# Performance work log

Hardware: AMD Instinct MI355X
Metric: run time of the kernel (lower is better)

## Reference

```python
import jax, jax.numpy as jnp
import numpy as np

ALPHA = 0.25
GAMMA = 1.5


def box_iou(a, b):
    # a: [A,4], b: [G,4] in xyxy; torchvision-style IoU
    area_a = (a[:, 2] - a[:, 0]) * (a[:, 3] - a[:, 1])  # [A]
    area_b = (b[:, 2] - b[:, 0]) * (b[:, 3] - b[:, 1])  # [G]
    lt = jnp.maximum(a[:, None, :2], b[None, :, :2])    # [A,G,2]
    rb = jnp.minimum(a[:, None, 2:], b[None, :, 2:])    # [A,G,2]
    wh = jnp.clip(rb - lt, 0.0)
    inter = wh[..., 0] * wh[..., 1]                      # [A,G]
    return inter / (area_a[:, None] + area_b[None, :] - inter)


def setup_inputs() -> dict:
    key = jax.random.key(0)
    ks = jax.random.split(key, 7)
    B, A, C, G = 8, 120000, 80, 32
    classifications = jax.random.uniform(ks[0], (B, A, C), minval=1e-4, maxval=1.0 - 1e-4, dtype=jnp.float32)
    regressions = jax.random.normal(ks[1], (B, A, 4), dtype=jnp.float32)
    actr = jax.random.uniform(ks[2], (A, 2), minval=0.0, maxval=512.0)
    awh = jax.random.uniform(ks[3], (A, 2), minval=16.0, maxval=128.0)
    anchors = jnp.concatenate([actr - 0.5 * awh, actr + 0.5 * awh], axis=-1)[None]  # [1,A,4]
    bctr = jax.random.uniform(ks[4], (B, G, 2), minval=0.0, maxval=512.0)
    bwh = jax.random.uniform(ks[5], (B, G, 2), minval=8.0, maxval=256.0)
    boxes = jnp.concatenate([bctr - 0.5 * bwh, bctr + 0.5 * bwh], axis=-1)  # [B,G,4]
    labels = jax.random.randint(ks[6], (B, G), 0, C, dtype=jnp.int32)
    return {"classifications": classifications, "regressions": regressions,
            "anchors": anchors, "boxes": boxes, "labels": labels}


def focal_loss(classifications, regressions, anchors, boxes, labels):
    anchor = anchors[0]                         # [A,4]
    num_classes = classifications.shape[-1]
    aw = anchor[:, 2] - anchor[:, 0]
    ah = anchor[:, 3] - anchor[:, 1]
    acx = anchor[:, 0] + 0.5 * aw
    acy = anchor[:, 1] + 0.5 * ah

    def per_sample(cls, reg, bx, lb):
        iou = box_iou(anchor, bx)               # [A,G]
        iou_max = jnp.max(iou, axis=1)
        iou_argmax = jnp.argmax(iou, axis=1)
        pos = iou_max >= 0.5                    # [A]
        num_pos = jnp.sum(pos.astype(cls.dtype))

        assigned = bx[iou_argmax]               # [A,4] gather
        onehot = jax.nn.one_hot(lb[iou_argmax], num_classes, dtype=cls.dtype)
        base = jnp.where(iou_max < 0.4, 0.0, -1.0)[:, None]  # ignore by default
        targets = jnp.where(pos[:, None], onehot, base)      # [A,C]

        alpha_factor = jnp.where(targets == 1.0, ALPHA, 1.0 - ALPHA)
        focal_weight = jnp.where(targets == 1.0, 1.0 - cls, cls)
        focal_weight = alpha_factor * focal_weight ** GAMMA
        bce = -(targets * jnp.log(jnp.clip(cls, 1e-6, 1.0))
                + (1.0 - targets) * jnp.log(jnp.clip(1.0 - cls, 1e-6, 1.0)))
        cls_loss = jnp.where(targets != -1.0, focal_weight * bce, 0.0)
        cls_loss = jnp.sum(cls_loss) / jnp.maximum(num_pos, 1.0)

        gw_raw = assigned[:, 2] - assigned[:, 0]
        gh_raw = assigned[:, 3] - assigned[:, 1]
        gcx = assigned[:, 0] + 0.5 * gw_raw
        gcy = assigned[:, 1] + 0.5 * gh_raw
        gw = jnp.clip(gw_raw, 1.0)
        gh = jnp.clip(gh_raw, 1.0)
        tdx = (gcx - acx) / aw
        tdy = (gcy - acy) / ah
        tdw = jnp.log(gw / aw)
        tdh = jnp.log(gh / ah)
        tgt = jnp.stack([tdx, tdy, tdw, tdh], axis=1)   # [A,4]
        diff = jnp.abs(tgt - reg)
        rl = jnp.where(diff <= 1.0 / 9.0, 0.5 * 9.0 * diff ** 2, diff - 0.5 / 9.0)
        # mean over positive anchors' 4 coords (0 if no positives)
        reg_loss = jnp.sum(rl * pos[:, None].astype(rl.dtype)) / (4.0 * jnp.maximum(num_pos, 1.0))
        return cls_loss, reg_loss

    cls_l, reg_l = jax.vmap(per_sample)(classifications, regressions, boxes, labels)
    return jnp.mean(cls_l, axis=0, keepdims=True), jnp.mean(reg_l, axis=0, keepdims=True)


def reference(classifications, regressions, anchors, boxes, labels):
    return focal_loss(classifications, regressions, anchors, boxes, labels)
```

## Files before the change

kernel.cpp:

```cpp
#include <hip/hip_runtime.h>
#include <math.h>

#define B_N 8
#define A_N 120000
#define C_N 80
#define G_N 32


__device__ __forceinline__ float smoothl1(float d) {
    return (d <= (1.0f / 9.0f)) ? 4.5f * d * d : d - (0.5f / 9.0f);
}

__device__ __forceinline__ float focal_term(float p, bool ispos) {
    float q  = 1.0f - p;
    float t  = ispos ? q : p;
    float lg = ispos ? p : q;
    float al = ispos ? 0.25f : 0.75f;
    return al * t * sqrtf(t) * (-__logf(fmaxf(lg, 1e-6f)));
}

__global__ void init_kernel(float* __restrict__ acc) {
    if (threadIdx.x < 24) acc[threadIdx.x] = 0.0f;
}

__global__ void assign_kernel(const float* __restrict__ anchors,
                              const float* __restrict__ regressions,
                              const float* __restrict__ boxes,
                              const int*   __restrict__ labels,
                              signed char* __restrict__ state,
                              float*       __restrict__ acc) {
    __shared__ float4 sbox[G_N];
    __shared__ int    slab[G_N];
    __shared__ float  sarea[G_N];
    __shared__ float2 sred[4];

    const int b   = blockIdx.y;
    const int tid = threadIdx.x;

    if (tid < G_N) {
        float4 bx = ((const float4*)boxes)[b * G_N + tid];
        sbox[tid]  = bx;
        slab[tid]  = labels[b * G_N + tid];
        sarea[tid] = (bx.z - bx.x) * (bx.w - bx.y);
    }
    __syncthreads();

    const int a = blockIdx.x * blockDim.x + tid;
    float my_reg = 0.0f;
    float my_pos = 0.0f;

    if (a < A_N) {
        float4 an = ((const float4*)anchors)[a];
        float area_a = (an.z - an.x) * (an.w - an.y);
        float best = -1.0f;
        int bestg = 0;
        #pragma unroll 8
        for (int g = 0; g < G_N; ++g) {
            float4 bx = sbox[g];
            float ltx = fmaxf(an.x, bx.x);
            float lty = fmaxf(an.y, bx.y);
            float rbx = fminf(an.z, bx.z);
            float rby = fminf(an.w, bx.w);
            float w = fmaxf(rbx - ltx, 0.0f);
            float h = fmaxf(rby - lty, 0.0f);
            float inter = w * h;
            float iou = inter / (area_a + sarea[g] - inter);
            if (iou > best) { best = iou; bestg = g; }
        }

        signed char st;
        if (best >= 0.5f) {
            st = (signed char)slab[bestg];
            my_pos = 1.0f;
            float4 bx = sbox[bestg];
            float aw  = an.z - an.x;
            float ah  = an.w - an.y;
            float acx = an.x + 0.5f * aw;
            float acy = an.y + 0.5f * ah;
            float gwr = bx.z - bx.x;
            float ghr = bx.w - bx.y;
            float gcx = bx.x + 0.5f * gwr;
            float gcy = bx.y + 0.5f * ghr;
            float gw  = fmaxf(gwr, 1.0f);
            float gh  = fmaxf(ghr, 1.0f);
            float t0 = (gcx - acx) / aw;
            float t1 = (gcy - acy) / ah;
            float t2 = __logf(gw / aw);
            float t3 = __logf(gh / ah);
            float4 rg = ((const float4*)regressions)[(size_t)b * A_N + a];
            my_reg = smoothl1(fabsf(t0 - rg.x)) + smoothl1(fabsf(t1 - rg.y))
                   + smoothl1(fabsf(t2 - rg.z)) + smoothl1(fabsf(t3 - rg.w));
        } else {
            st = (best < 0.4f) ? (signed char)(-2) : (signed char)(-1);
        }
        state[(size_t)b * A_N + a] = st;
    }

    #pragma unroll
    for (int off = 32; off > 0; off >>= 1) {
        my_reg += __shfl_down(my_reg, off);
        my_pos += __shfl_down(my_pos, off);
    }
    if ((tid & 63) == 0) sred[tid >> 6] = make_float2(my_reg, my_pos);
    __syncthreads();
    if (tid == 0) {
        float r = sred[0].x + sred[1].x + sred[2].x + sred[3].x;
        float p = sred[0].y + sred[1].y + sred[2].y + sred[3].y;
        atomicAdd(&acc[8 + b],  r);
        atomicAdd(&acc[16 + b], p);
    }
}

__global__ void cls_kernel(const float*       __restrict__ cls,
                           const signed char* __restrict__ state,
                           float*             __restrict__ acc) {
    __shared__ float sred[4];
    const int b = blockIdx.y;
    const float4*      p  = (const float4*)(cls + (size_t)b * A_N * C_N);
    const signed char* st = state + (size_t)b * A_N;

    const int n4 = A_N * C_N / 4;
    float sum = 0.0f;
    for (int i = blockIdx.x * blockDim.x + threadIdx.x; i < n4;
         i += gridDim.x * blockDim.x) {
        int a     = i / 20;
        int cbase = (i - a * 20) * 4;
        int s = st[a];
        if (s == -1) continue;
        float4 v = p[i];
        sum += focal_term(v.x, s == cbase);
        sum += focal_term(v.y, s == cbase + 1);
        sum += focal_term(v.z, s == cbase + 2);
        sum += focal_term(v.w, s == cbase + 3);
    }

    #pragma unroll
    for (int off = 32; off > 0; off >>= 1) sum += __shfl_down(sum, off);
    if ((threadIdx.x & 63) == 0) sred[threadIdx.x >> 6] = sum;
    __syncthreads();
    if (threadIdx.x == 0) {
        atomicAdd(&acc[b], sred[0] + sred[1] + sred[2] + sred[3]);
    }
}

__global__ void finalize_kernel(const float* __restrict__ acc,
                                float*       __restrict__ out) {
    if (threadIdx.x == 0 && blockIdx.x == 0) {
        float cl = 0.0f, rl = 0.0f;
        #pragma unroll
        for (int b = 0; b < B_N; ++b) {
            float np = fmaxf(acc[16 + b], 1.0f);
            cl += acc[b] / np;
            rl += acc[8 + b] / (4.0f * np);
        }
        out[0] = cl * (1.0f / B_N);
        out[1] = rl * (1.0f / B_N);
    }
}

extern "C" void kernel_launch(void* const* d_in, const int* in_sizes, int n_in,
                              void* d_out, int out_size, void* d_ws, size_t ws_size,
                              hipStream_t stream) {
    const float* cls = (const float*)d_in[0];
    const float* reg = (const float*)d_in[1];
    const float* anc = (const float*)d_in[2];
    const float* box = (const float*)d_in[3];
    const int*   lab = (const int*)d_in[4];
    float* out = (float*)d_out;

    float*       acc   = (float*)d_ws;
    signed char* state = (signed char*)d_ws + 128;

    hipLaunchKernelGGL(init_kernel, dim3(1), dim3(32), 0, stream, acc);

    dim3 g1((A_N + 255) / 256, B_N);
    hipLaunchKernelGGL(assign_kernel, g1, dim3(256), 0, stream,
                       anc, reg, box, lab, state, acc);

    dim3 g2(1200, B_N);
    hipLaunchKernelGGL(cls_kernel, g2, dim3(256), 0, stream, cls, state, acc);

    hipLaunchKernelGGL(finalize_kernel, dim3(1), dim3(64), 0, stream, acc, out);
}
```

Baseline: 517.3 us.

## Fuse anchor assignment and classification focal loss into one kernel

Merges the IoU assignment kernel and the classification loss kernel so each block assigns its 256 anchors, keeps their states in shared memory, then streams the matching classification rows. This removes the global state buffer round trip and one kernel launch. The cls pass loses its grid-stride schedule and now runs a fixed 20 iterations per block, with the IoU work in front of it in the same block.

```diff
diff --git a/kernel.cpp b/kernel.cpp
--- a/kernel.cpp
+++ b/kernel.cpp
@@ -23,19 +23,23 @@
     if (threadIdx.x < 24) acc[threadIdx.x] = 0.0f;
 }
 
-__global__ void assign_kernel(const float* __restrict__ anchors,
-                              const float* __restrict__ regressions,
-                              const float* __restrict__ boxes,
-                              const int*   __restrict__ labels,
-                              signed char* __restrict__ state,
-                              float*       __restrict__ acc) {
-    __shared__ float4 sbox[G_N];
-    __shared__ int    slab[G_N];
-    __shared__ float  sarea[G_N];
-    __shared__ float2 sred[4];
+__global__ __launch_bounds__(256) void fused_kernel(
+        const float* __restrict__ anchors,
+        const float* __restrict__ regressions,
+        const float* __restrict__ cls,
+        const float* __restrict__ boxes,
+        const int*   __restrict__ labels,
+        float*       __restrict__ acc) {
+    __shared__ float4      sbox[G_N];
+    __shared__ int         slab[G_N];
+    __shared__ float       sarea[G_N];
+    __shared__ signed char sstate[256];
+    __shared__ float2      sred2[4];
+    __shared__ float       sred[4];
 
-    const int b   = blockIdx.y;
-    const int tid = threadIdx.x;
+    const int b      = blockIdx.y;
+    const int tid    = threadIdx.x;
+    const int base_a = blockIdx.x << 8;
 
     if (tid < G_N) {
         float4 bx = ((const float4*)boxes)[b * G_N + tid];
@@ -45,9 +49,10 @@
     }
     __syncthreads();
 
-    const int a = blockIdx.x * blockDim.x + tid;
+    const int a = base_a + tid;
     float my_reg = 0.0f;
     float my_pos = 0.0f;
+    signed char st = -1;
 
     if (a < A_N) {
         float4 an = ((const float4*)anchors)[a];
@@ -68,7 +73,6 @@
             if (iou > best) { best = iou; bestg = g; }
         }
 
-        signed char st;
         if (best >= 0.5f) {
             st = (signed char)slab[bestg];
             my_pos = 1.0f;
@@ -93,41 +97,34 @@
         } else {
             st = (best < 0.4f) ? (signed char)(-2) : (signed char)(-1);
         }
-        state[(size_t)b * A_N + a] = st;
     }
+    sstate[tid] = st;
 
     #pragma unroll
     for (int off = 32; off > 0; off >>= 1) {
         my_reg += __shfl_down(my_reg, off);
         my_pos += __shfl_down(my_pos, off);
     }
-    if ((tid & 63) == 0) sred[tid >> 6] = make_float2(my_reg, my_pos);
+    if ((tid & 63) == 0) sred2[tid >> 6] = make_float2(my_reg, my_pos);
     __syncthreads();
     if (tid == 0) {
-        float r = sred[0].x + sred[1].x + sred[2].x + sred[3].x;
-        float p = sred[0].y + sred[1].y + sred[2].y + sred[3].y;
+        float r = sred2[0].x + sred2[1].x + sred2[2].x + sred2[3].x;
+        float p = sred2[0].y + sred2[1].y + sred2[2].y + sred2[3].y;
         atomicAdd(&acc[8 + b],  r);
         atomicAdd(&acc[16 + b], p);
     }
-}
 
-__global__ void cls_kernel(const float*       __restrict__ cls,
-                           const signed char* __restrict__ state,
-                           float*             __restrict__ acc) {
-    __shared__ float sred[4];
-    const int b = blockIdx.y;
-    const float4*      p  = (const float4*)(cls + (size_t)b * A_N * C_N);
-    const signed char* st = state + (size_t)b * A_N;
+    const int n_anch = min(256, A_N - base_a);
+    const int n4 = n_anch * 20;
+    const float4* p4 = (const float4*)(cls + (size_t)b * A_N * C_N) + (size_t)base_a * 20;
 
-    const int n4 = A_N * C_N / 4;
     float sum = 0.0f;
-    for (int i = blockIdx.x * blockDim.x + threadIdx.x; i < n4;
-         i += gridDim.x * blockDim.x) {
-        int a     = i / 20;
-        int cbase = (i - a * 20) * 4;
-        int s = st[a];
+    for (int i = tid; i < n4; i += 256) {
+        int al    = i / 20;
+        int cbase = (i - al * 20) * 4;
+        int s = sstate[al];
         if (s == -1) continue;
-        float4 v = p[i];
+        float4 v = p4[i];
         sum += focal_term(v.x, s == cbase);
         sum += focal_term(v.y, s == cbase + 1);
         sum += focal_term(v.z, s == cbase + 2);
@@ -136,9 +133,9 @@
 
     #pragma unroll
     for (int off = 32; off > 0; off >>= 1) sum += __shfl_down(sum, off);
-    if ((threadIdx.x & 63) == 0) sred[threadIdx.x >> 6] = sum;
+    if ((tid & 63) == 0) sred[tid >> 6] = sum;
     __syncthreads();
-    if (threadIdx.x == 0) {
+    if (tid == 0) {
         atomicAdd(&acc[b], sred[0] + sred[1] + sred[2] + sred[3]);
     }
 }
@@ -168,17 +165,13 @@
     const int*   lab = (const int*)d_in[4];
     float* out = (float*)d_out;
 
-    float*       acc   = (float*)d_ws;
-    signed char* state = (signed char*)d_ws + 128;
+    float* acc = (float*)d_ws;
 
     hipLaunchKernelGGL(init_kernel, dim3(1), dim3(32), 0, stream, acc);
 
-    dim3 g1((A_N + 255) / 256, B_N);
-    hipLaunchKernelGGL(assign_kernel, g1, dim3(256), 0, stream,
-                       anc, reg, box, lab, state, acc);
-
-    dim3 g2(1200, B_N);
-    hipLaunchKernelGGL(cls_kernel, g2, dim3(256), 0, stream, cls, state, acc);
+    dim3 g((A_N + 255) / 256, B_N);
+    hipLaunchKernelGGL(fused_kernel, g, dim3(256), 0, stream,
+                       anc, reg, cls, box, lab, acc);
 
     hipLaunchKernelGGL(finalize_kernel, dim3(1), dim3(64), 0, stream, acc, out);
 }
```

After: 461.3 us. 10.8% less time.
